# Performance work log

Measured on AMD Instinct MI355X. Metric: run time of the kernel, lower is better.

The kernel has to match this reference:

```python
import jax, jax.numpy as jnp
import numpy as np

B, L, D, N = 2, 2048, 1024, 16
DT = 0.1  # liquid scaler integration step


def setup_inputs() -> dict:
    key = jax.random.key(0)
    ks = jax.random.split(key, 10)
    def w(k, shape, scale=0.02):
        return jax.random.normal(k, shape, jnp.float32) * scale
    log_min, log_max = float(np.log(0.001)), float(np.log(0.1))
    dt_bias = jax.random.uniform(ks[1], (D,), jnp.float32) * (log_max - log_min) + log_min
    return {
        "x": jax.random.normal(ks[0], (B, L, D), jnp.float32),
        "delta_W": w(ks[2], (D, D)), "delta_b": jnp.zeros((D,), jnp.float32),
        "B_W": w(ks[3], (N, D)), "B_b": jnp.zeros((N,), jnp.float32),
        "C_W": w(ks[4], (N, D)), "C_b": jnp.zeros((N,), jnp.float32),
        "A_log": jnp.zeros((D, N), jnp.float32),
        "dt_bias": dt_bias,
        "tau": jnp.ones((N,), jnp.float32),
        "Wi_W": w(ks[5], (N, D)), "Wi_b": jnp.zeros((N,), jnp.float32),
        "Wr_W": w(ks[6], (N, N)),
        "sel_W": w(ks[7], (D, N)), "sel_b": jnp.zeros((D,), jnp.float32),
        "h0": jnp.zeros((1, N), jnp.float32),
    }


def reference(x, delta_W, delta_b, B_W, B_b, C_W, C_b, A_log, dt_bias, tau,
              Wi_W, Wi_b, Wr_W, sel_W, sel_b, h0):
    Bsz, Ls, Dm = x.shape
    Ns = A_log.shape[1]

    # --- LiquidTimeConstantScaler ---
    gc = x.mean(axis=1)                                # [B, D]
    inp_sig = gc @ Wi_W.T + Wi_b                       # [B, N]
    cur = jnp.broadcast_to(h0, (Bsz, Ns))              # [B, N]
    rec = cur @ Wr_W.T                                 # [B, N]
    tau_c = jnp.clip(tau, 0.1, 10.0)
    dh_dt = (-cur + jnp.tanh(inp_sig + rec)) / tau_c[None, :]
    new_h = cur + DT * dh_dt                           # [B, N]
    sel = jax.nn.sigmoid(new_h @ sel_W.T + sel_b)      # [B, D]
    xs = x * sel[:, None, :]                           # [B, L, D]

    # --- selective SSM discretization ---
    delta = jax.nn.softplus(xs @ delta_W.T + delta_b + dt_bias)  # [B, L, D]
    Bm = xs @ B_W.T + B_b                              # [B, L, N]
    Cm = xs @ C_W.T + C_b                              # [B, L, N]
    A = -jnp.exp(A_log)                                # [D, N]
    A_d = jnp.exp(A[None, None] * delta[..., None])    # [B, L, D, N]
    factor = jnp.where(jnp.abs(A)[None, None] < 1e-6,
                       delta[..., None], (A_d - 1.0) / A[None, None])
    B_d = factor * Bm[:, :, None, :]                   # [B, L, D, N]

    # --- linear recurrence over time via scan ---
    def step(h, inputs):
        Ad_t, Bd_t, x_t, C_t = inputs                  # [B,D,N],[B,D,N],[B,D],[B,N]
        h = Ad_t * h + Bd_t * x_t[..., None]
        y = jnp.einsum('bdn,bn->bd', h, C_t)
        return h, y

    h_init = jnp.zeros((Bsz, Dm, Ns), x.dtype)
    _, ys = jax.lax.scan(step, h_init,
                         (A_d.transpose(1, 0, 2, 3), B_d.transpose(1, 0, 2, 3),
                          xs.transpose(1, 0, 2), Cm.transpose(1, 0, 2)))
    return ys.transpose(1, 0, 2)                        # [B, L, D]
```

## Files before the change

kernel.cpp:

```cpp
#include <hip/hip_runtime.h>
#include <hip/hip_bf16.h>
#include <math.h>

#define B_ 2
#define L_ 2048
#define D_ 1024
#define N_ 16
#define CCH 64
#define TCH 32
#define NCOLS 1056
#define NPAD  1088

typedef unsigned short u16;
typedef __attribute__((ext_vector_type(8))) short short8v;
typedef __attribute__((ext_vector_type(8))) unsigned short ushort8v;
typedef __attribute__((ext_vector_type(4))) float f32x4;

__device__ __forceinline__ float softplusf(float z) {
  return fmaxf(z, 0.f) + log1pf(__expf(-fabsf(z)));
}

__device__ __forceinline__ u16 bf16rne(float f) {
  union { float f; unsigned u; } c; c.f = f;
  unsigned u = c.u;
  u += 0x7fffu + ((u >> 16) & 1u);
  return (u16)(u >> 16);
}

__device__ __forceinline__ void gl_lds16(const void* g, const u16* lds_base,
                                         int byte_off) {
  byte_off = __builtin_amdgcn_readfirstlane(byte_off);
  __builtin_amdgcn_global_load_lds(
      (const __attribute__((address_space(1))) void*)g,
      (__attribute__((address_space(3))) void*)((const char*)lds_base + byte_off),
      16, 0, 0);
}

__global__ __launch_bounds__(256) void k_gc_pack(const float* __restrict__ x,
    float* __restrict__ part1, u16* __restrict__ xb) {
  int blk = blockIdx.x;
  int b = blk >> 8, lc = blk & 255;
  int tid = threadIdx.x;
  int r0 = b * L_ + lc * 8;
  float4 s = {0.f, 0.f, 0.f, 0.f};
  #pragma unroll
  for (int q = 0; q < 8; ++q) {
    size_t off = (size_t)(r0 + q) * D_ + tid * 4;
    float4 v = *(const float4*)(x + off);
    s.x += v.x; s.y += v.y; s.z += v.z; s.w += v.w;
    ushort4 r;
    r.x = bf16rne(v.x); r.y = bf16rne(v.y);
    r.z = bf16rne(v.z); r.w = bf16rne(v.w);
    *(ushort4*)(xb + off) = r;
  }
  *(float4*)(part1 + (size_t)blk * D_ + tid * 4) = s;
}

__global__ __launch_bounds__(256) void k_gc_red(const float* __restrict__ part1,
                                                float* __restrict__ part2) {
  int gid = blockIdx.x * 256 + threadIdx.x;
  int d = gid & 1023;
  int jc = (gid >> 10) & 15;
  int b = gid >> 14;
  float s = 0.f;
  #pragma unroll
  for (int t = 0; t < 16; ++t)
    s += part1[(size_t)(b * 256 + jc * 16 + t) * D_ + d];
  part2[gid] = s;
}

__global__ __launch_bounds__(256) void k_newh(const float* __restrict__ part2,
    const float* __restrict__ Wi_W, const float* __restrict__ Wi_b,
    const float* __restrict__ Wr_W, const float* __restrict__ tau,
    const float* __restrict__ h0, float* __restrict__ newh) {
  __shared__ float gcs[B_ * D_];
  int tid = threadIdx.x;
  for (int idx = tid; idx < B_ * D_; idx += 256) {
    int b = idx >> 10, d = idx & (D_ - 1);
    float s = 0.f;
    #pragma unroll
    for (int lc = 0; lc < 16; ++lc)
      s += part2[(size_t)((b << 4) | lc) * D_ + d];
    gcs[idx] = s * (1.f / L_);
  }
  __syncthreads();
  if (tid < B_ * N_) {
    int b = tid >> 4, n = tid & 15;
    float inp = Wi_b[n];
    const float* g = gcs + b * D_;
    const float* w = Wi_W + n * D_;
    for (int d = 0; d < D_; d += 4) {
      float4 gv = *(const float4*)(g + d);
      float4 wv = *(const float4*)(w + d);
      inp += gv.x * wv.x + gv.y * wv.y + gv.z * wv.z + gv.w * wv.w;
    }
    float rec = 0.f;
    for (int m = 0; m < N_; ++m) rec += h0[m] * Wr_W[n * N_ + m];
    float th = tanhf(inp + rec);
    float tc = fminf(fmaxf(tau[n], 0.1f), 10.f);
    float cur = h0[n];
    newh[tid] = cur + 0.1f * ((th - cur) / tc);
  }
}

__global__ __launch_bounds__(256) void k_sel(const float* __restrict__ newh,
    const float* __restrict__ sel_W, const float* __restrict__ sel_b,
    float* __restrict__ sel) {
  int gid = blockIdx.x * 256 + threadIdx.x;
  int b = gid >> 10, d = gid & (D_ - 1);
  const float* w = sel_W + d * N_;
  const float* h = newh + b * N_;
  float z = sel_b[d];
  #pragma unroll
  for (int n = 0; n < N_; n += 4) {
    float4 wv = *(const float4*)(w + n);
    z += h[n] * wv.x + h[n + 1] * wv.y + h[n + 2] * wv.z + h[n + 3] * wv.w;
  }
  sel[gid] = 1.f / (1.f + __expf(-z));
}

__global__ __launch_bounds__(256) void k_pack_w(const float* __restrict__ dW,
    const float* __restrict__ B_W, const float* __restrict__ C_W,
    const float* __restrict__ sel, u16* __restrict__ Wp) {
  int gid = blockIdx.x * 256 + threadIdx.x;
  int b = blockIdx.y;
  size_t e = (size_t)gid * 8;
  int nn = (int)(e >> 10);
  int k = (int)(e & 1023);
  ushort8v r;
  if (nn < NCOLS) {
    const float* src = (nn < 1024) ? dW + (size_t)nn * 1024
                     : (nn < 1040) ? B_W + (size_t)(nn - 1024) * 1024
                                   : C_W + (size_t)(nn - 1040) * 1024;
    float4 s0 = *(const float4*)(src + k);
    float4 s1 = *(const float4*)(src + k + 4);
    const float* sp = sel + b * D_ + k;
    float4 e0 = *(const float4*)sp;
    float4 e1 = *(const float4*)(sp + 4);
    r[0] = bf16rne(s0.x * e0.x); r[1] = bf16rne(s0.y * e0.y);
    r[2] = bf16rne(s0.z * e0.z); r[3] = bf16rne(s0.w * e0.w);
    r[4] = bf16rne(s1.x * e1.x); r[5] = bf16rne(s1.y * e1.y);
    r[6] = bf16rne(s1.z * e1.z); r[7] = bf16rne(s1.w * e1.w);
  } else {
    r = (ushort8v)0;
  }
  *(ushort8v*)(Wp + (size_t)b * (NPAD * 1024) + e) = r;
}

__global__ __launch_bounds__(256) void k_gemm(
    const u16* __restrict__ xb, const u16* __restrict__ Wp,
    const float* __restrict__ delta_b, const float* __restrict__ dt_bias,
    const float* __restrict__ B_b, const float* __restrict__ C_b,
    float* __restrict__ delta, float* __restrict__ Bm, float* __restrict__ Cm) {
  __shared__ __align__(16) u16 lds[4][4096];
  int m0 = blockIdx.x * 64;
  int n0 = blockIdx.y * 64;
  int batch = blockIdx.x >> 5;
  const u16* wb = Wp + (size_t)batch * (NPAD * 1024);
  int tid = threadIdx.x;
  int w = tid >> 6, l = tid & 63;
  int wr = w >> 1, wc = w & 1;
  int srow = l >> 3;
  int ssl = (l & 7) ^ srow;

  f32x4 acc[2][2];
  #pragma unroll
  for (int m = 0; m < 2; ++m)
    #pragma unroll
    for (int n = 0; n < 2; ++n)
      acc[m][n] = (f32x4){0.f, 0.f, 0.f, 0.f};

  #define STAGE(kb, buf)                                                       \
    {                                                                          \
      _Pragma("unroll")                                                        \
      for (int q = 0; q < 2; ++q) {                                            \
        int row = w * 16 + q * 8 + srow;                                       \
        gl_lds16(xb + (size_t)(m0 + row) * 1024 + (kb) * 64 + ssl * 8,         \
                 &lds[0][0], (buf) * 8192 + (w * 16 + q * 8) * 128);           \
        gl_lds16(wb + (size_t)(n0 + row) * 1024 + (kb) * 64 + ssl * 8,         \
                 &lds[0][0], 16384 + (buf) * 8192 + (w * 16 + q * 8) * 128);   \
      }                                                                        \
    }

  int lr = l & 15, lh = l >> 4;

  #define CSTEP(cur)                                                           \
    {                                                                          \
      _Pragma("unroll")                                                        \
      for (int ks = 0; ks < 2; ++ks) {                                         \
        short8v a[2], bq[2];                                                   \
        _Pragma("unroll")                                                      \
        for (int m = 0; m < 2; ++m) {                                          \
          int r = wr * 32 + m * 16 + lr;                                       \
          int ps = (ks * 4 + lh) ^ (r & 7);                                    \
          a[m] = *(const short8v*)((const char*)&lds[0][0] + (cur) * 8192 + r * 128 + ps * 16);\
        }                                                                      \
        _Pragma("unroll")                                                      \
        for (int n = 0; n < 2; ++n) {                                          \
          int r = wc * 32 + n * 16 + lr;                                       \
          int ps = (ks * 4 + lh) ^ (r & 7);                                    \
          bq[n] = *(const short8v*)((const char*)&lds[0][0] + 16384 + (cur) * 8192 + r * 128 + ps * 16);\
        }                                                                      \
        _Pragma("unroll")                                                      \
        for (int m = 0; m < 2; ++m)                                            \
          _Pragma("unroll")                                                    \
          for (int n = 0; n < 2; ++n)                                          \
            acc[m][n] = __builtin_amdgcn_mfma_f32_16x16x32_bf16(a[m], bq[n],   \
                                                                acc[m][n], 0, 0, 0);\
      }                                                                        \
    }

  STAGE(0, 0);
  STAGE(1, 1);
  #pragma unroll
  for (int kb = 0; kb < 15; ++kb) {
    int cur = kb & 1;
    asm volatile("s_waitcnt vmcnt(4)" ::: "memory");
    __builtin_amdgcn_s_barrier();
    CSTEP(cur);
    asm volatile("s_waitcnt lgkmcnt(0)" ::: "memory");
    __builtin_amdgcn_s_barrier();
    if (kb < 14) STAGE(kb + 2, cur);
  }
  asm volatile("s_waitcnt vmcnt(0)" ::: "memory");
  __builtin_amdgcn_s_barrier();
  CSTEP(1);
  #undef STAGE
  #undef CSTEP

  int ibase = m0 + wr * 32 + lh * 4;
  int jbase = n0 + wc * 32 + lr;
  #pragma unroll
  for (int m = 0; m < 2; ++m) {
    #pragma unroll
    for (int n = 0; n < 2; ++n) {
      int j = jbase + n * 16;
      #pragma unroll
      for (int r = 0; r < 2 * 2; ++r) {
        int i = ibase + m * 16 + r;
        float v = acc[m][n][r];
        if (j < 1024) {
          delta[(size_t)i * D_ + j] = softplusf(v + delta_b[j] + dt_bias[j]);
        } else if (j < 1040) {
          Bm[i * N_ + (j - 1024)] = v + B_b[j - 1024];
        } else if (j < NCOLS) {
          Cm[i * N_ + (j - 1040)] = v + C_b[j - 1040];
        }
      }
    }
  }
}

__global__ __launch_bounds__(256) void k_scan1(const float* __restrict__ x,
    const float* __restrict__ sel, const float* __restrict__ delta,
    const float* __restrict__ Bm, const float* __restrict__ A_log,
    float* __restrict__ prodA, float* __restrict__ hend) {
  int gid = blockIdx.x * 256 + threadIdx.x;
  int nq = gid & 3;
  int d = (gid >> 2) & (D_ - 1);
  int c = (gid >> 12) & (CCH - 1);
  int b = gid >> 18;
  float A[4], rA[4];
  unsigned smallm = 0;
  {
    float4 a0 = *(const float4*)(A_log + d * N_ + nq * 4);
    float av[4] = {a0.x, a0.y, a0.z, a0.w};
    #pragma unroll
    for (int n = 0; n < 4; ++n) {
      float a = -__expf(av[n]);
      A[n] = a; rA[n] = 1.f / a;
      if (fabsf(a) < 1e-6f) smallm |= (1u << n);
    }
  }
  float selv = sel[b * D_ + d];
  float h[4], p[4];
  #pragma unroll
  for (int n = 0; n < 4; ++n) { h[n] = 0.f; p[n] = 1.f; }
  int row0 = b * L_ + c * TCH;
  const float* xp = x + (size_t)row0 * D_ + d;
  const float* dp = delta + (size_t)row0 * D_ + d;
  const float4* bmp = (const float4*)(Bm + (size_t)row0 * N_) + nq;
  #pragma unroll 4
  for (int s = 0; s < TCH; ++s) {
    float dlt = dp[(size_t)s * D_];
    float xv = xp[(size_t)s * D_] * selv;
    float4 q0 = bmp[s * 4];
    float bmv[4] = {q0.x, q0.y, q0.z, q0.w};
    #pragma unroll
    for (int n = 0; n < 4; ++n) {
      float Ad = __expf(A[n] * dlt);
      float f = ((smallm >> n) & 1u) ? dlt : (Ad - 1.f) * rA[n];
      h[n] = Ad * h[n] + (f * bmv[n]) * xv;
      p[n] *= Ad;
    }
  }
  size_t base = ((size_t)(gid >> 2)) * N_ + nq * 4;
  *(float4*)(prodA + base) = make_float4(p[0], p[1], p[2], p[3]);
  *(float4*)(hend + base)  = make_float4(h[0], h[1], h[2], h[3]);
}

__global__ __launch_bounds__(256) void k_scan2(const float* __restrict__ prodA,
    const float* __restrict__ hend, float* __restrict__ hin) {
  int gid = blockIdx.x * 256 + threadIdx.x;
  int b = gid >> 14;
  int rem = gid & 16383;
  size_t base = ((size_t)(b * CCH) << 14) + rem;
  float H = 0.f;
  #pragma unroll
  for (int g = 0; g < 4; ++g) {
    float pg[16], hg[16];
    #pragma unroll
    for (int t = 0; t < 16; ++t) {
      size_t idx = base + ((size_t)(g * 16 + t) << 14);
      pg[t] = prodA[idx];
      hg[t] = hend[idx];
    }
    #pragma unroll
    for (int t = 0; t < 16; ++t) {
      size_t idx = base + ((size_t)(g * 16 + t) << 14);
      hin[idx] = H;
      H = pg[t] * H + hg[t];
    }
  }
}

__global__ __launch_bounds__(256) void k_scan3(const float* __restrict__ x,
    const float* __restrict__ sel, const float* __restrict__ delta,
    const float* __restrict__ Bm, const float* __restrict__ Cm,
    const float* __restrict__ A_log, const float* __restrict__ hin,
    float* __restrict__ out) {
  int gid = blockIdx.x * 256 + threadIdx.x;
  int nq = gid & 3;
  int d = (gid >> 2) & (D_ - 1);
  int c = (gid >> 12) & (CCH - 1);
  int b = gid >> 18;
  float A[4], rA[4];
  unsigned smallm = 0;
  {
    float4 a0 = *(const float4*)(A_log + d * N_ + nq * 4);
    float av[4] = {a0.x, a0.y, a0.z, a0.w};
    #pragma unroll
    for (int n = 0; n < 4; ++n) {
      float a = -__expf(av[n]);
      A[n] = a; rA[n] = 1.f / a;
      if (fabsf(a) < 1e-6f) smallm |= (1u << n);
    }
  }
  float selv = sel[b * D_ + d];
  float h[4];
  {
    size_t base = ((size_t)(gid >> 2)) * N_ + nq * 4;
    float4 v0 = *(const float4*)(hin + base);
    h[0] = v0.x; h[1] = v0.y; h[2] = v0.z; h[3] = v0.w;
  }
  int row0 = b * L_ + c * TCH;
  const float* xp = x + (size_t)row0 * D_ + d;
  const float* dp = delta + (size_t)row0 * D_ + d;
  const float4* bmp = (const float4*)(Bm + (size_t)row0 * N_) + nq;
  const float4* cmp = (const float4*)(Cm + (size_t)row0 * N_) + nq;
  float* op = out + (size_t)row0 * D_ + d;
  #pragma unroll 4
  for (int s = 0; s < TCH; ++s) {
    float dlt = dp[(size_t)s * D_];
    float xv = xp[(size_t)s * D_] * selv;
    float4 q0 = bmp[s * 4];
    float4 r0 = cmp[s * 4];
    float bmv[4] = {q0.x, q0.y, q0.z, q0.w};
    float cmv[4] = {r0.x, r0.y, r0.z, r0.w};
    float yp = 0.f;
    #pragma unroll
    for (int n = 0; n < 4; ++n) {
      float Ad = __expf(A[n] * dlt);
      float f = ((smallm >> n) & 1u) ? dlt : (Ad - 1.f) * rA[n];
      h[n] = Ad * h[n] + (f * bmv[n]) * xv;
      yp += h[n] * cmv[n];
    }
    float y = yp + __shfl_xor(yp, 1, 64);
    y += __shfl_xor(y, 2, 64);
    if (nq == 0) op[(size_t)s * D_] = y;
  }
}

extern "C" void kernel_launch(void* const* d_in, const int* in_sizes, int n_in,
                              void* d_out, int out_size, void* d_ws, size_t ws_size,
                              hipStream_t stream) {
  const float* x       = (const float*)d_in[0];
  const float* deltaW  = (const float*)d_in[1];
  const float* deltab  = (const float*)d_in[2];
  const float* B_W     = (const float*)d_in[3];
  const float* B_b     = (const float*)d_in[4];
  const float* C_W     = (const float*)d_in[5];
  const float* C_b     = (const float*)d_in[6];
  const float* A_log   = (const float*)d_in[7];
  const float* dt_bias = (const float*)d_in[8];
  const float* tau     = (const float*)d_in[9];
  const float* Wi_W    = (const float*)d_in[10];
  const float* Wi_b    = (const float*)d_in[11];
  const float* Wr_W    = (const float*)d_in[12];
  const float* sel_W   = (const float*)d_in[13];
  const float* sel_b   = (const float*)d_in[14];
  const float* h0      = (const float*)d_in[15];
  float* out = (float*)d_out;

  float* ws    = (float*)d_ws;
  float* delta = ws;
  float* newh  = delta + 4194304;
  float* selp  = newh + 64;
  float* Bm    = selp + 2048;
  float* Cm    = Bm + 65536;
  float* prodA = Cm + 65536;
  float* hend  = prodA + 2097152;
  float* hin   = hend + 2097152;
  u16* xb    = (u16*)prodA;
  u16* Wp    = (u16*)hend;
  float* part1 = hin;
  float* part2 = hin + 524288;

  hipLaunchKernelGGL(k_gc_pack, dim3(512), dim3(256), 0, stream, x, part1, xb);
  hipLaunchKernelGGL(k_gc_red, dim3(128), dim3(256), 0, stream, part1, part2);
  hipLaunchKernelGGL(k_newh, dim3(1), dim3(256), 0, stream,
                     part2, Wi_W, Wi_b, Wr_W, tau, h0, newh);
  hipLaunchKernelGGL(k_sel, dim3(8), dim3(256), 0, stream,
                     newh, sel_W, sel_b, selp);
  hipLaunchKernelGGL(k_pack_w, dim3(544, 2), dim3(256), 0, stream,
                     deltaW, B_W, C_W, selp, Wp);
  hipLaunchKernelGGL(k_gemm, dim3(64, 17), dim3(256), 0, stream,
                     xb, Wp, deltab, dt_bias, B_b, C_b, delta, Bm, Cm);
  hipLaunchKernelGGL(k_scan1, dim3(2048), dim3(256), 0, stream,
                     x, selp, delta, Bm, A_log, prodA, hend);
  hipLaunchKernelGGL(k_scan2, dim3(128), dim3(256), 0, stream,
                     prodA, hend, hin);
  hipLaunchKernelGGL(k_scan3, dim3(2048), dim3(256), 0, stream,
                     x, selp, delta, Bm, Cm, A_log, hin, out);
}
```

Before: 130.0 us.

## Read bf16 x in scans, fuse newh/sel kernels, swizzle GEMM tile order

```diff
diff --git a/kernel.cpp b/kernel.cpp
--- a/kernel.cpp
+++ b/kernel.cpp
@@ -27,6 +27,12 @@
   return (u16)(u >> 16);
 }
 
+__device__ __forceinline__ float bf16tof(u16 v) {
+  union { unsigned u; float f; } c;
+  c.u = (unsigned)v << 16;
+  return c.f;
+}
+
 __device__ __forceinline__ void gl_lds16(const void* g, const u16* lds_base,
                                          int byte_off) {
   byte_off = __builtin_amdgcn_readfirstlane(byte_off);
@@ -69,11 +75,13 @@
   part2[gid] = s;
 }
 
-__global__ __launch_bounds__(256) void k_newh(const float* __restrict__ part2,
+__global__ __launch_bounds__(256) void k_newh_sel(const float* __restrict__ part2,
     const float* __restrict__ Wi_W, const float* __restrict__ Wi_b,
     const float* __restrict__ Wr_W, const float* __restrict__ tau,
-    const float* __restrict__ h0, float* __restrict__ newh) {
+    const float* __restrict__ h0, const float* __restrict__ sel_W,
+    const float* __restrict__ sel_b, float* __restrict__ selp) {
   __shared__ float gcs[B_ * D_];
+  __shared__ float nh[B_ * N_];
   int tid = threadIdx.x;
   for (int idx = tid; idx < B_ * D_; idx += 256) {
     int b = idx >> 10, d = idx & (D_ - 1);
@@ -99,24 +107,21 @@
     float th = tanhf(inp + rec);
     float tc = fminf(fmaxf(tau[n], 0.1f), 10.f);
     float cur = h0[n];
-    newh[tid] = cur + 0.1f * ((th - cur) / tc);
-  }
-}
-
-__global__ __launch_bounds__(256) void k_sel(const float* __restrict__ newh,
-    const float* __restrict__ sel_W, const float* __restrict__ sel_b,
-    float* __restrict__ sel) {
-  int gid = blockIdx.x * 256 + threadIdx.x;
-  int b = gid >> 10, d = gid & (D_ - 1);
-  const float* w = sel_W + d * N_;
-  const float* h = newh + b * N_;
-  float z = sel_b[d];
-  #pragma unroll
-  for (int n = 0; n < N_; n += 4) {
-    float4 wv = *(const float4*)(w + n);
-    z += h[n] * wv.x + h[n + 1] * wv.y + h[n + 2] * wv.z + h[n + 3] * wv.w;
-  }
-  sel[gid] = 1.f / (1.f + __expf(-z));
+    nh[tid] = cur + 0.1f * ((th - cur) / tc);
+  }
+  __syncthreads();
+  for (int i = tid; i < B_ * D_; i += 256) {
+    int b = i >> 10, d = i & (D_ - 1);
+    const float* w = sel_W + d * N_;
+    const float* h = nh + b * N_;
+    float z = sel_b[d];
+    #pragma unroll
+    for (int n = 0; n < N_; n += 4) {
+      float4 wv = *(const float4*)(w + n);
+      z += h[n] * wv.x + h[n + 1] * wv.y + h[n + 2] * wv.z + h[n + 3] * wv.w;
+    }
+    selp[i] = 1.f / (1.f + __expf(-z));
+  }
 }
 
 __global__ __launch_bounds__(256) void k_pack_w(const float* __restrict__ dW,
@@ -153,9 +158,12 @@
     const float* __restrict__ B_b, const float* __restrict__ C_b,
     float* __restrict__ delta, float* __restrict__ Bm, float* __restrict__ Cm) {
   __shared__ __align__(16) u16 lds[4][4096];
-  int m0 = blockIdx.x * 64;
-  int n0 = blockIdx.y * 64;
-  int batch = blockIdx.x >> 5;
+  int wgid = blockIdx.y * 64 + blockIdx.x;
+  int swz = (wgid & 7) * 136 + (wgid >> 3);
+  int mx = swz & 63, ny = swz >> 6;
+  int m0 = mx * 64;
+  int n0 = ny * 64;
+  int batch = mx >> 5;
   const u16* wb = Wp + (size_t)batch * (NPAD * 1024);
   int tid = threadIdx.x;
   int w = tid >> 6, l = tid & 63;
@@ -251,7 +259,7 @@
   }
 }
 
-__global__ __launch_bounds__(256) void k_scan1(const float* __restrict__ x,
+__global__ __launch_bounds__(256) void k_scan1(const u16* __restrict__ xb,
     const float* __restrict__ sel, const float* __restrict__ delta,
     const float* __restrict__ Bm, const float* __restrict__ A_log,
     float* __restrict__ prodA, float* __restrict__ hend) {
@@ -277,13 +285,13 @@
   #pragma unroll
   for (int n = 0; n < 4; ++n) { h[n] = 0.f; p[n] = 1.f; }
   int row0 = b * L_ + c * TCH;
-  const float* xp = x + (size_t)row0 * D_ + d;
+  const u16* xp = xb + (size_t)row0 * D_ + d;
   const float* dp = delta + (size_t)row0 * D_ + d;
   const float4* bmp = (const float4*)(Bm + (size_t)row0 * N_) + nq;
   #pragma unroll 4
   for (int s = 0; s < TCH; ++s) {
     float dlt = dp[(size_t)s * D_];
-    float xv = xp[(size_t)s * D_] * selv;
+    float xv = bf16tof(xp[(size_t)s * D_]) * selv;
     float4 q0 = bmp[s * 4];
     float bmv[4] = {q0.x, q0.y, q0.z, q0.w};
     #pragma unroll
@@ -324,7 +332,7 @@
   }
 }
 
-__global__ __launch_bounds__(256) void k_scan3(const float* __restrict__ x,
+__global__ __launch_bounds__(256) void k_scan3(const u16* __restrict__ xb,
     const float* __restrict__ sel, const float* __restrict__ delta,
     const float* __restrict__ Bm, const float* __restrict__ Cm,
     const float* __restrict__ A_log, const float* __restrict__ hin,
@@ -354,7 +362,7 @@
     h[0] = v0.x; h[1] = v0.y; h[2] = v0.z; h[3] = v0.w;
   }
   int row0 = b * L_ + c * TCH;
-  const float* xp = x + (size_t)row0 * D_ + d;
+  const u16* xp = xb + (size_t)row0 * D_ + d;
   const float* dp = delta + (size_t)row0 * D_ + d;
   const float4* bmp = (const float4*)(Bm + (size_t)row0 * N_) + nq;
   const float4* cmp = (const float4*)(Cm + (size_t)row0 * N_) + nq;
@@ -362,7 +370,7 @@
   #pragma unroll 4
   for (int s = 0; s < TCH; ++s) {
     float dlt = dp[(size_t)s * D_];
-    float xv = xp[(size_t)s * D_] * selv;
+    float xv = bf16tof(xp[(size_t)s * D_]) * selv;
     float4 q0 = bmp[s * 4];
     float4 r0 = cmp[s * 4];
     float bmv[4] = {q0.x, q0.y, q0.z, q0.w};
@@ -404,32 +412,29 @@
 
   float* ws    = (float*)d_ws;
   float* delta = ws;
-  float* newh  = delta + 4194304;
-  float* selp  = newh + 64;
+  float* selp  = delta + 4194304;
   float* Bm    = selp + 2048;
   float* Cm    = Bm + 65536;
-  float* prodA = Cm + 65536;
-  float* hend  = prodA + 2097152;
-  float* hin   = hend + 2097152;
-  u16* xb    = (u16*)prodA;
-  u16* Wp    = (u16*)hend;
+  u16*   xb    = (u16*)(Cm + 65536);
+  u16*   Wp    = xb + 4194304;
+  float* hin   = (float*)(Wp + 2228224);
   float* part1 = hin;
   float* part2 = hin + 524288;
+  float* prodA = out;
+  float* hend  = out + 2097152;
 
   hipLaunchKernelGGL(k_gc_pack, dim3(512), dim3(256), 0, stream, x, part1, xb);
   hipLaunchKernelGGL(k_gc_red, dim3(128), dim3(256), 0, stream, part1, part2);
-  hipLaunchKernelGGL(k_newh, dim3(1), dim3(256), 0, stream,
-                     part2, Wi_W, Wi_b, Wr_W, tau, h0, newh);
-  hipLaunchKernelGGL(k_sel, dim3(8), dim3(256), 0, stream,
-                     newh, sel_W, sel_b, selp);
+  hipLaunchKernelGGL(k_newh_sel, dim3(1), dim3(256), 0, stream,
+                     part2, Wi_W, Wi_b, Wr_W, tau, h0, sel_W, sel_b, selp);
   hipLaunchKernelGGL(k_pack_w, dim3(544, 2), dim3(256), 0, stream,
                      deltaW, B_W, C_W, selp, Wp);
   hipLaunchKernelGGL(k_gemm, dim3(64, 17), dim3(256), 0, stream,
                      xb, Wp, deltab, dt_bias, B_b, C_b, delta, Bm, Cm);
   hipLaunchKernelGGL(k_scan1, dim3(2048), dim3(256), 0, stream,
-                     x, selp, delta, Bm, A_log, prodA, hend);
+                     xb, selp, delta, Bm, A_log, prodA, hend);
   hipLaunchKernelGGL(k_scan2, dim3(128), dim3(256), 0, stream,
                      prodA, hend, hin);
   hipLaunchKernelGGL(k_scan3, dim3(2048), dim3(256), 0, stream,
-                     x, selp, delta, Bm, Cm, A_log, hin, out);
-}
+                     xb, selp, delta, Bm, Cm, A_log, hin, out);
+}
```

Measured after the change: 139.1 us. +7.0%, slower.
